# Kernel optimization log

Measured on AMD Instinct MI355X. Metric: run time of the kernel, lower is better.

The kernel has to match this reference:

```python
import jax, jax.numpy as jnp
import numpy as np

K = 11          # kernel_size
SIGMA = 1.5
CH = 3          # image channels


def _gaussian_kernel(ch):
    coords = jnp.arange(K, dtype=jnp.float32) - (K - 1) / 2
    g = jnp.exp(-coords ** 2 / (2 * SIGMA ** 2))
    g = g / g.sum()
    k2d = jnp.outer(g, g)                       # [K, K]
    return jnp.tile(k2d[None, None], (ch, 1, 1, 1))  # [C, 1, K, K] depthwise


def setup_inputs() -> dict:
    key = jax.random.key(0)
    kx, ky = jax.random.split(key)
    x = jax.random.normal(kx, (32, CH, 512, 512), dtype=jnp.float32)
    y = jax.random.normal(ky, (32, CH, 512, 512), dtype=jnp.float32)
    kernel = _gaussian_kernel(CH)
    return {"x": x, "y": y, "kernel": kernel}


def _blur(v, kernel):
    # depthwise 2D Gaussian blur, SAME padding (K odd)
    c = v.shape[1]
    pad = K // 2
    return jax.lax.conv_general_dilated(
        v, kernel, window_strides=(1, 1), padding=[(pad, pad), (pad, pad)],
        dimension_numbers=("NCHW", "OIHW", "NCHW"), feature_group_count=c)


def reference(x, y, kernel):
    C1 = 0.01 ** 2
    C2 = 0.03 ** 2
    mu_x = _blur(x, kernel)
    mu_y = _blur(y, kernel)
    sigma_x = _blur(x * x, kernel) - mu_x ** 2
    sigma_y = _blur(y * y, kernel) - mu_y ** 2
    sigma_xy = _blur(x * y, kernel) - mu_x * mu_y
    ssim_num = (2 * mu_x * mu_y + C1) * (2 * sigma_xy + C2)
    ssim_den = (mu_x ** 2 + mu_y ** 2 + C1) * (sigma_x + sigma_y + C2)
    ssim = ssim_num / (ssim_den + 1e-8)
    return ((1.0 - ssim) / 2.0).mean()
```

## Files before the change

kernel.cpp:

```cpp
#include <hip/hip_runtime.h>
#include <hip/hip_bf16.h>

#define IMG    512
#define KSZ    11
#define PANEL  16
#define STRIP  64
#define FS     20
#define CS     84
#define WRSZ   (16 * CS)

typedef short bf16x8 __attribute__((ext_vector_type(8)));
typedef float f32x4  __attribute__((ext_vector_type(4)));
union S8 { bf16x8 v; ushort u16[8]; uint u32[4]; };

__device__ __forceinline__ uint cvtpk(float lo, float hi) {
    uint r;
    asm("v_cvt_pk_bf16_f32 %0, %1, %2" : "=v"(r) : "v"(lo), "v"(hi));
    return r;
}
__device__ __forceinline__ float2 pk_mul(float2 a, float2 b) {
    float2 d;
    asm("v_pk_mul_f32 %0, %1, %2" : "=v"(d) : "v"(a), "v"(b));
    return d;
}
__device__ __forceinline__ float2 pk_add(float2 a, float2 b) {
    float2 d;
    asm("v_pk_add_f32 %0, %1, %2" : "=v"(d) : "v"(a), "v"(b));
    return d;
}
__device__ __forceinline__ float2 pk_fma(float2 a, float2 b, float2 c) {
    float2 d;
    asm("v_pk_fma_f32 %0, %1, %2, %3" : "=v"(d) : "v"(a), "v"(b), "v"(c));
    return d;
}
__device__ __forceinline__ ushort f2bf(float f) {
    union { __hip_bfloat16 h; ushort u; } c;
    c.h = __float2bfloat16(f);
    return c.u;
}


__global__ __launch_bounds__(256)
void dssim_mfma_kernel(const float* __restrict__ x,
                       const float* __restrict__ y,
                       const float* __restrict__ kern,
                       float* __restrict__ out)
{
    __shared__ float  sgf[16];
    __shared__ ushort gext[64];
    __shared__ __align__(16) uint Wring[4 * WRSZ];
    __shared__ float  wsum[4];

    const int tid = threadIdx.x;
    const int l   = tid & 63;
    const int wv  = tid >> 6;
    const int q   = l >> 4;
    const int cj  = l & 15;
    const int wb  = wv * WRSZ;

    if (tid < KSZ) {
        float s = 0.f;
        #pragma unroll
        for (int j = 0; j < KSZ; ++j) s += kern[tid * KSZ + j];
        sgf[tid] = s;
    }
    for (int i = l; i < 256; i += 64) {
        const int col = i >> 4, r = i & 15, f = r >> 2, p = r & 3;
        Wring[wb + col * CS + f * FS + p] = 0u;
    }
    __syncthreads();
    if (tid < 64) {
        const int d = tid - 18;
        gext[tid] = (d >= 0 && d < KSZ) ? f2bf(sgf[d]) : (ushort)0;
    }
    __syncthreads();

    S8 tg;
    #pragma unroll
    for (int ii = 0; ii < 8; ++ii)
        tg.u16[ii] = gext[15 + q * 8 + ii - cj];

    const int plane  = blockIdx.z;
    const int half   = blockIdx.y;
    const int cstrip = blockIdx.x * STRIP;
    const int base   = plane * (IMG * IMG);

    const int  cb    = cstrip - 8 + 16 * wv + 8 * q;
    const bool colok = (cb >= 0) && (cb + 8 <= IMG);
    const float* xl  = x + base + cb + cj * IMG;
    const float* yl  = y + base + cb + cj * IMG;

    const int t0    = half ? 15 : 0;
    const int t1    = half ? 32 : 16;
    const int hreal = half ? 31 : 16;
    const int vmin  = half ? 17 : 1;

    const f32x4 z0 = {0.f, 0.f, 0.f, 0.f};
    const float C1 = 1e-4f, C2 = 9e-4f;
    const float2 m1 = make_float2(-1.f, -1.f);
    float local = 0.f;
    const int colbase = wb + cj * CS;

    int hg = (2 * t0 + 1 + (q >> 1)) % 5;
    int vg = (2 * t0 - 2 + q + 10) % 5;
    const int ho = 2 * (q & 1);

    f32x4 xa0, xb0, ya0, yb0, xa1, xb1, ya1, yb1;

    auto load8 = [&](int t, f32x4& xa, f32x4& xb, f32x4& ya, f32x4& yb) {
        const float* px = xl + t * (PANEL * IMG);
        const float* py = yl + t * (PANEL * IMG);
        if (colok) {
            xa = *(const f32x4*)px;  xb = *(const f32x4*)(px + 4);
            ya = *(const f32x4*)py;  yb = *(const f32x4*)(py + 4);
        } else {
            xa = z0; xb = z0; ya = z0; yb = z0;
        }
    };

    auto step = [&](int t, f32x4& xa, f32x4& xb, f32x4& ya, f32x4& yb) {
        const int hw = colbase + hg * 4 + ho;
        if (t <= hreal) {
            S8 fs, fd, fP, fM;
            #pragma unroll
            for (int w = 0; w < 4; ++w) {
                const float2 xv = (w == 0) ? make_float2(xa[0], xa[1])
                                : (w == 1) ? make_float2(xa[2], xa[3])
                                : (w == 2) ? make_float2(xb[0], xb[1])
                                :            make_float2(xb[2], xb[3]);
                const float2 yv = (w == 0) ? make_float2(ya[0], ya[1])
                                : (w == 1) ? make_float2(ya[2], ya[3])
                                : (w == 2) ? make_float2(yb[0], yb[1])
                                :            make_float2(yb[2], yb[3]);
                const float2 sv = pk_add(xv, yv);
                const float2 dv = pk_fma(yv, m1, xv);
                const float2 Pv = pk_mul(sv, sv);
                const float2 Mv = pk_mul(dv, dv);
                fs.u32[w] = cvtpk(sv.x, sv.y);
                fd.u32[w] = cvtpk(dv.x, dv.y);
                fP.u32[w] = cvtpk(Pv.x, Pv.y);
                fM.u32[w] = cvtpk(Mv.x, Mv.y);
            }

            if (t + 2 <= hreal) load8(t + 2, xa, xb, ya, yb);

            f32x4 d;
            uint2 w2;
            d = __builtin_amdgcn_mfma_f32_16x16x32_bf16(fs.v, tg.v, z0, 0, 0, 0);
            w2.x = cvtpk(d[0], d[1]);  w2.y = cvtpk(d[2], d[3]);
            *(uint2*)&Wring[hw + 0 * FS] = w2;
            d = __builtin_amdgcn_mfma_f32_16x16x32_bf16(fd.v, tg.v, z0, 0, 0, 0);
            w2.x = cvtpk(d[0], d[1]);  w2.y = cvtpk(d[2], d[3]);
            *(uint2*)&Wring[hw + 1 * FS] = w2;
            d = __builtin_amdgcn_mfma_f32_16x16x32_bf16(fP.v, tg.v, z0, 0, 0, 0);
            w2.x = cvtpk(d[0], d[1]);  w2.y = cvtpk(d[2], d[3]);
            *(uint2*)&Wring[hw + 2 * FS] = w2;
            d = __builtin_amdgcn_mfma_f32_16x16x32_bf16(fM.v, tg.v, z0, 0, 0, 0);
            w2.x = cvtpk(d[0], d[1]);  w2.y = cvtpk(d[2], d[3]);
            *(uint2*)&Wring[hw + 3 * FS] = w2;
        } else {
            const uint2 zz = {0u, 0u};
            #pragma unroll
            for (int f = 0; f < 4; ++f) *(uint2*)&Wring[hw + f * FS] = zz;
        }

        if (t >= vmin) {
            const int vr = colbase + vg * 4;
            f32x4 vf[4];
            #pragma unroll
            for (int f = 0; f < 4; ++f) {
                const uint4 bb = *(const uint4*)&Wring[vr + f * FS];
                S8 b;
                b.u32[0] = bb.x; b.u32[1] = bb.y; b.u32[2] = bb.z; b.u32[3] = bb.w;
                vf[f] = __builtin_amdgcn_mfma_f32_16x16x32_bf16(tg.v, b.v, z0, 0, 0, 0);
            }
            #pragma unroll
            for (int r = 0; r < 4; ++r) {
                const float us = vf[0][r], ud = vf[1][r];
                const float P  = vf[2][r], M  = vf[3][r];
                const float u  = us * us, v = ud * ud;
                const float a  = fmaf(0.5f, u - v, C1);
                const float b  = fmaf(0.5f, u + v, C1);
                const float ps = P - u,  md = M - v;
                const float c  = fmaf(0.5f, ps - md, C2);
                const float e  = fmaf(0.5f, ps + md, C2);
                local += __fdividef(a * c, fmaf(b, e, 1e-8f));
            }
        }

        hg += 2;  if (hg >= 5) hg -= 5;
        vg += 2;  if (vg >= 5) vg -= 5;
    };

    load8(t0,     xa0, xb0, ya0, yb0);
    load8(t0 + 1, xa1, xb1, ya1, yb1);

    for (int tt = t0; tt <= t1; tt += 2) {
        step(tt, xa0, xb0, ya0, yb0);
        if (tt + 1 <= t1) step(tt + 1, xa1, xb1, ya1, yb1);
    }

    #pragma unroll
    for (int o = 32; o > 0; o >>= 1) local += __shfl_down(local, o, 64);
    if (l == 0) wsum[wv] = local;
    __syncthreads();
    if (tid == 0) {
        const float ssimsum = wsum[0] + wsum[1] + wsum[2] + wsum[3];
        atomicAdd(out, (16384.f - ssimsum) * (0.5f / 25165824.f));
    }
}

extern "C" void kernel_launch(void* const* d_in, const int* in_sizes, int n_in,
                              void* d_out, int out_size, void* d_ws, size_t ws_size,
                              hipStream_t stream)
{
    const float* x    = (const float*)d_in[0];
    const float* y    = (const float*)d_in[1];
    const float* kern = (const float*)d_in[2];
    float* out = (float*)d_out;

    hipMemsetAsync(out, 0, sizeof(float), stream);

    dim3 grid(IMG / STRIP, 2, 32 * 3);
    dssim_mfma_kernel<<<grid, 256, 0, stream>>>(x, y, kern, out);
}
```

Before: 76.04 us.

## Stage input panels through LDS with global_load_lds instead of register double-buffer

Replaces the two-deep register prefetch of x/y panel rows with direct global-to-LDS loads into a per-wave staging buffer. Each step waits on vmcnt(0), reads its data from LDS, then issues the load for the next panel. This frees registers and shortens the prefetch depth from two panels to one. The cost is extra LDS traffic and a full memory wait every step, which may expose load latency.

```diff
diff --git a/kernel.cpp b/kernel.cpp
--- a/kernel.cpp
+++ b/kernel.cpp
@@ -12,6 +12,11 @@
 typedef short bf16x8 __attribute__((ext_vector_type(8)));
 typedef float f32x4  __attribute__((ext_vector_type(4)));
 union S8 { bf16x8 v; ushort u16[8]; uint u32[4]; };
+union U4 { uint4 u; float f[4]; };
+
+#define GLL(g, s) __builtin_amdgcn_global_load_lds( \
+    (const __attribute__((address_space(1))) void*)(g), \
+    (__attribute__((address_space(3))) void*)(s), 16, 0, 0)
 
 __device__ __forceinline__ uint cvtpk(float lo, float hi) {
     uint r;
@@ -48,7 +53,8 @@
 {
     __shared__ float  sgf[16];
     __shared__ ushort gext[64];
-    __shared__ __align__(16) uint Wring[4 * WRSZ];
+    __shared__ __align__(16) uint  Wring[4 * WRSZ];
+    __shared__ __align__(16) uint4 Stage[4][2][2][64];
     __shared__ float  wsum[4];
 
     const int tid = threadIdx.x;
@@ -68,6 +74,8 @@
         const int col = i >> 4, r = i & 15, f = r >> 2, p = r & 3;
         Wring[wb + col * CS + f * FS + p] = 0u;
     }
+    for (int i = tid; i < 4 * 2 * 2 * 64; i += 256)
+        ((uint4*)Stage)[i] = make_uint4(0u, 0u, 0u, 0u);
     __syncthreads();
     if (tid < 64) {
         const int d = tid - 18;
@@ -105,33 +113,37 @@
     int vg = (2 * t0 - 2 + q + 10) % 5;
     const int ho = 2 * (q & 1);
 
-    f32x4 xa0, xb0, ya0, yb0, xa1, xb1, ya1, yb1;
-
-    auto load8 = [&](int t, f32x4& xa, f32x4& xb, f32x4& ya, f32x4& yb) {
+    auto issue_stage = [&](int t) {
         const float* px = xl + t * (PANEL * IMG);
         const float* py = yl + t * (PANEL * IMG);
         if (colok) {
-            xa = *(const f32x4*)px;  xb = *(const f32x4*)(px + 4);
-            ya = *(const f32x4*)py;  yb = *(const f32x4*)(py + 4);
-        } else {
-            xa = z0; xb = z0; ya = z0; yb = z0;
+            GLL(px,     &Stage[wv][0][0][0]);
+            GLL(px + 4, &Stage[wv][0][1][0]);
+            GLL(py,     &Stage[wv][1][0][0]);
+            GLL(py + 4, &Stage[wv][1][1][0]);
         }
     };
 
-    auto step = [&](int t, f32x4& xa, f32x4& xb, f32x4& ya, f32x4& yb) {
+    auto step = [&](int t) {
         const int hw = colbase + hg * 4 + ho;
         if (t <= hreal) {
+            asm volatile("s_waitcnt vmcnt(0)" ::: "memory");
+            __builtin_amdgcn_sched_barrier(0);
+            U4 XA, XB, YA, YB;
+            XA.u = Stage[wv][0][0][l];
+            XB.u = Stage[wv][0][1][l];
+            YA.u = Stage[wv][1][0][l];
+            YB.u = Stage[wv][1][1][l];
+
             S8 fs, fd, fP, fM;
             #pragma unroll
             for (int w = 0; w < 4; ++w) {
-                const float2 xv = (w == 0) ? make_float2(xa[0], xa[1])
-                                : (w == 1) ? make_float2(xa[2], xa[3])
-                                : (w == 2) ? make_float2(xb[0], xb[1])
-                                :            make_float2(xb[2], xb[3]);
-                const float2 yv = (w == 0) ? make_float2(ya[0], ya[1])
-                                : (w == 1) ? make_float2(ya[2], ya[3])
-                                : (w == 2) ? make_float2(yb[0], yb[1])
-                                :            make_float2(yb[2], yb[3]);
+                const float2 xv = (w < 2)
+                    ? make_float2(XA.f[2 * w], XA.f[2 * w + 1])
+                    : make_float2(XB.f[2 * (w - 2)], XB.f[2 * (w - 2) + 1]);
+                const float2 yv = (w < 2)
+                    ? make_float2(YA.f[2 * w], YA.f[2 * w + 1])
+                    : make_float2(YB.f[2 * (w - 2)], YB.f[2 * (w - 2) + 1]);
                 const float2 sv = pk_add(xv, yv);
                 const float2 dv = pk_fma(yv, m1, xv);
                 const float2 Pv = pk_mul(sv, sv);
@@ -142,7 +154,7 @@
                 fM.u32[w] = cvtpk(Mv.x, Mv.y);
             }
 
-            if (t + 2 <= hreal) load8(t + 2, xa, xb, ya, yb);
+            if (t + 1 <= hreal) issue_stage(t + 1);
 
             f32x4 d;
             uint2 w2;
@@ -192,13 +204,8 @@
         vg += 2;  if (vg >= 5) vg -= 5;
     };
 
-    load8(t0,     xa0, xb0, ya0, yb0);
-    load8(t0 + 1, xa1, xb1, ya1, yb1);
-
-    for (int tt = t0; tt <= t1; tt += 2) {
-        step(tt, xa0, xb0, ya0, yb0);
-        if (tt + 1 <= t1) step(tt + 1, xa1, xb1, ya1, yb1);
-    }
+    issue_stage(t0);
+    for (int t = t0; t <= t1; ++t) step(t);
 
     #pragma unroll
     for (int o = 32; o > 0; o >>= 1) local += __shfl_down(local, o, 64);
```

Measured after the change: 81.73 us. 7.5% more time.
